# Kernel tuning notes

Hardware: AMD Instinct MI355X
Metric: run time of the kernel (lower is better)

## Reference

```python
import jax, jax.numpy as jnp
import numpy as np
import math

N_HEAD = 16


def setup_inputs() -> dict:
    key = jax.random.key(0)
    ks = jax.random.split(key, 4)
    B, S, D = 4, 2048, 1024
    x = jax.random.normal(ks[0], (B, S, D), dtype=jnp.float32)
    c_attn_w = jax.random.normal(ks[1], (D, 3 * D), dtype=jnp.float32) * 0.02
    c_attn_b = jnp.zeros((3 * D,), dtype=jnp.float32)
    c_proj_w = jax.random.normal(ks[2], (D, D), dtype=jnp.float32) * 0.02
    c_proj_b = jnp.zeros((D,), dtype=jnp.float32)
    # causal mask: True where attention is disallowed (future positions)
    mask_self_attention = jnp.triu(jnp.ones((S, S), dtype=bool), k=1)[None, None]
    return {"x": x, "c_attn_w": c_attn_w, "c_attn_b": c_attn_b,
            "c_proj_w": c_proj_w, "c_proj_b": c_proj_b,
            "mask_self_attention": mask_self_attention}


def reference(x, c_attn_w, c_attn_b, c_proj_w, c_proj_b, mask_self_attention):
    B, S, D = x.shape
    H = N_HEAD
    hd = D // H
    qkv = x @ c_attn_w + c_attn_b                      # [B,S,3D]
    q, k, v = jnp.split(qkv, 3, axis=-1)
    # split heads -> [B,H,S,hd]
    q = q.reshape(B, S, H, hd).transpose(0, 2, 1, 3)
    k = k.reshape(B, S, H, hd).transpose(0, 2, 1, 3)
    v = v.reshape(B, S, H, hd).transpose(0, 2, 1, 3)
    w = jnp.einsum('bhqd,bhkd->bhqk', q, k) / math.sqrt(hd)  # scale=True
    w = jnp.where(mask_self_attention, jnp.float32(-10000.0), w)
    w = jax.nn.softmax(w, axis=-1)
    a = jnp.einsum('bhqk,bhkd->bhqd', w, v)            # [B,H,S,hd]
    a = a.transpose(0, 2, 1, 3).reshape(B, S, D)       # merge heads
    return a @ c_proj_w + c_proj_b
```

## Files before the change

### kernel.cpp

```cpp
#include <hip/hip_runtime.h>
#include <cstdint>
#include <cstddef>

#define S_LEN 2048
#define D_MODEL 1024
#define HD 64

typedef __attribute__((ext_vector_type(8))) __bf16 bf16x8;
typedef __attribute__((ext_vector_type(8))) unsigned short u16x8;
typedef __attribute__((ext_vector_type(4))) float f32x4;
typedef __attribute__((ext_vector_type(4))) unsigned short u16x4;

static __device__ __forceinline__ unsigned short f32_bf16(float f) {
    unsigned int u = __float_as_uint(f);
    u += 0x7fffu + ((u >> 16) & 1u);
    return (unsigned short)(u >> 16);
}

static __device__ __forceinline__ unsigned short f32_bf16_rn(float f) {
    return __builtin_bit_cast(unsigned short, (__bf16)f);
}

static __device__ __forceinline__ float fast_exp2(float x) {
#if __has_builtin(__builtin_amdgcn_exp2f)
    return __builtin_amdgcn_exp2f(x);
#else
    float r; asm("v_exp_f32 %0, %1" : "=v"(r) : "v"(x)); return r;
#endif
}

static __device__ __forceinline__ void gload_lds16(const void* g, void* l) {
    __builtin_amdgcn_global_load_lds(
        (const __attribute__((address_space(1))) unsigned int*)g,
        (__attribute__((address_space(3))) unsigned int*)l,
        16, 0, 0);
}

static __device__ __forceinline__ bf16x8 frag8(const unsigned short* p) {
    return __builtin_bit_cast(bf16x8, *(const u16x8*)p);
}

__global__ void prep_k(const float* __restrict__ x, unsigned short* __restrict__ xb,
                       const float* __restrict__ caw, unsigned short* __restrict__ wqt,
                       const float* __restrict__ cpw, unsigned short* __restrict__ wpt)
{
    __shared__ float tile[32][33];
    const int blk = blockIdx.x;
    const int tid = threadIdx.x;
    if (blk < 8192) {
        int i = blk * 256 + tid;
        f32x4 v = ((const f32x4*)x)[i];
        u16x4 o;
        o[0] = f32_bf16(v[0]); o[1] = f32_bf16(v[1]);
        o[2] = f32_bf16(v[2]); o[3] = f32_bf16(v[3]);
        ((u16x4*)xb)[i] = o;
        return;
    }
    const float* in; unsigned short* out; int R, C, bx, by;
    if (blk < 11264) {
        int t = blk - 8192; in = caw; out = wqt; R = 1024; C = 3072;
        bx = t % 96; by = t / 96;
    } else {
        int t = blk - 11264; in = cpw; out = wpt; R = 1024; C = 1024;
        bx = t & 31; by = t >> 5;
    }
    int tx = tid & 31, ty = tid >> 5;
    int x0 = bx * 32, y0 = by * 32;
#pragma unroll
    for (int p = 0; p < 32; p += 8)
        tile[ty + p][tx] = in[(size_t)(y0 + ty + p) * C + x0 + tx];
    __syncthreads();
#pragma unroll
    for (int p = 0; p < 32; p += 8)
        out[(size_t)(x0 + ty + p) * R + y0 + tx] = f32_bf16(tile[tx][ty + p]);
}

__device__ __forceinline__ void gemm128_mainloop(
    const unsigned short* __restrict__ A,
    const unsigned short* __restrict__ Bt,
    unsigned short* As, unsigned short* Bs,
    int m0, int n0, int Kdim, f32x4 acc[][4])
{
    const int tid = threadIdx.x;
    const int lane = tid & 63, wave = tid >> 6;
    const int wm = wave & 1, wn = wave >> 1;
    const int quad = lane >> 4, l15 = lane & 15;
    const int srow = wave * 8 + (lane >> 3);
    const int scol = ((lane & 7) ^ (lane >> 3)) * 8;
    const unsigned short* Ag = A + (size_t)(m0 + srow) * Kdim + scol;
    const unsigned short* Bg = Bt + (size_t)(n0 + srow) * Kdim + scol;
    unsigned short* Asw = As + (wave * 8) * 64 + lane * 8;
    unsigned short* Bsw = Bs + (wave * 8) * 64 + lane * 8;
    const int mkey = l15 & 7;

    for (int k0 = 0; k0 < Kdim; k0 += 64) {
        __syncthreads();
#pragma unroll
        for (int p = 0; p < 4; ++p)
            gload_lds16(Ag + (size_t)(p * 32) * Kdim + k0, Asw + (p * 32) * 64);
#pragma unroll
        for (int p = 0; p < 4; ++p)
            gload_lds16(Bg + (size_t)(p * 32) * Kdim + k0, Bsw + (p * 32) * 64);
        __syncthreads();
#pragma unroll
        for (int kh = 0; kh < 2; ++kh) {
            bf16x8 af[4], bfv[4];
#pragma unroll
            for (int i = 0; i < 4; ++i)
                af[i] = frag8(As + (wm * 64 + i * 16 + l15) * 64 +
                              ((((kh << 2) + quad) ^ mkey) << 3));
#pragma unroll
            for (int j = 0; j < 4; ++j)
                bfv[j] = frag8(Bs + (wn * 64 + j * 16 + l15) * 64 +
                               ((((kh << 2) + quad) ^ mkey) << 3));
#pragma unroll
            for (int i = 0; i < 4; ++i)
#pragma unroll
                for (int j = 0; j < 4; ++j)
                    acc[i][j] = __builtin_amdgcn_mfma_f32_16x16x32_bf16(
                        af[i], bfv[j], acc[i][j], 0, 0, 0);
        }
    }
}

__global__ __launch_bounds__(256, 2) void gemm_qkv_k(
    const unsigned short* __restrict__ xb,
    const unsigned short* __restrict__ wt,
    const float* __restrict__ bias,
    unsigned short* __restrict__ q,
    unsigned short* __restrict__ k2,
    unsigned short* __restrict__ vt)
{
    __shared__ unsigned short Sh[128 * 132];
    unsigned short* As = Sh;
    unsigned short* Bs = Sh + 128 * 64;
    const int lin = blockIdx.x + 24 * blockIdx.y;
    const int swz = (lin & 7) * 192 + (lin >> 3);
    const int n0 = (swz % 24) * 128, m0 = (swz / 24) * 128;
    f32x4 acc[4][4] = {};
    gemm128_mainloop(xb, wt, As, Bs, m0, n0, 1024, acc);

    const int tid = threadIdx.x;
    const int lane = tid & 63, wave = tid >> 6;
    const int wm = wave & 1, wn = wave >> 1;
    const int quad = lane >> 4, l15 = lane & 15;
    const bool isq = (n0 < 1024);
    const bool isv = (n0 >= 2048);
    const int cb = n0 & 1023;

    if (!isv) {
        unsigned short* outp = isq ? q : k2;
#pragma unroll
        for (int j = 0; j < 4; ++j) {
            int ct = cb + wn * 64 + j * 16 + l15;
            int h = ct >> 6, d = ct & 63;
            float bv = bias[n0 + wn * 64 + j * 16 + l15];
#pragma unroll
            for (int i = 0; i < 4; ++i)
#pragma unroll
                for (int r = 0; r < 4; ++r) {
                    int row = m0 + wm * 64 + i * 16 + quad * 4 + r;
                    int bb = row >> 11, s = row & 2047;
                    float val = acc[i][j][r] + bv;
                    if (isq) val *= 0.1803368801111244f;
                    outp[((size_t)(bb * 16 + h) * S_LEN + s) * HD + d] = f32_bf16(val);
                }
        }
    } else {
        __syncthreads();
#pragma unroll
        for (int j = 0; j < 4; ++j) {
            float bv = bias[n0 + wn * 64 + j * 16 + l15];
            int lc = wn * 64 + j * 16 + l15;
#pragma unroll
            for (int i = 0; i < 4; ++i)
#pragma unroll
                for (int r = 0; r < 4; ++r) {
                    int lr = wm * 64 + i * 16 + quad * 4 + r;
                    Sh[lr * 132 + lc] = f32_bf16(acc[i][j][r] + bv);
                }
        }
        __syncthreads();
        const int lc = (tid & 63) + (wave & 1) * 64;
        const int sh2 = wave >> 1;
        const int bb = m0 >> 11;
        const int s0 = (m0 & 2047) + sh2 * 64;
        const int bh = bb * 16 + (cb >> 6) + (lc >> 6);
        unsigned short* vp = vt + ((size_t)bh * HD + (lc & 63)) * S_LEN + s0;
#pragma unroll
        for (int k8 = 0; k8 < 8; ++k8) {
            u16x8 w;
#pragma unroll
            for (int e = 0; e < 8; ++e)
                w[e] = Sh[(sh2 * 64 + k8 * 8 + e) * 132 + lc];
            *(u16x8*)(vp + k8 * 8) = w;
        }
    }
}

__global__ __launch_bounds__(256, 2) void gemm_proj_k(
    const unsigned short* __restrict__ am,
    const unsigned short* __restrict__ wpt,
    const float* __restrict__ bias,
    float* __restrict__ out)
{
    __shared__ unsigned short As[128 * 64], Bs[128 * 64];
    const int lin = blockIdx.x + 8 * blockIdx.y;
    const int swz = (lin & 7) * 64 + (lin >> 3);
    const int n0 = (swz % 8) * 128, m0 = (swz / 8) * 128;
    f32x4 acc[4][4] = {};
    gemm128_mainloop(am, wpt, As, Bs, m0, n0, 1024, acc);

    const int lane = threadIdx.x & 63, wave = threadIdx.x >> 6;
    const int wm = wave & 1, wn = wave >> 1;
    const int quad = lane >> 4, l15 = lane & 15;
#pragma unroll
    for (int j = 0; j < 4; ++j) {
        int col = n0 + wn * 64 + j * 16 + l15;
        float bv = bias[col];
#pragma unroll
        for (int i = 0; i < 4; ++i)
#pragma unroll
            for (int r = 0; r < 4; ++r) {
                int row = m0 + wm * 64 + i * 16 + quad * 4 + r;
                out[(size_t)row * 1024 + col] = acc[i][j][r] + bv;
            }
    }
}

#define PSTR 72
__global__ __launch_bounds__(256, 2) void flash_attn_k(
    const unsigned short* __restrict__ Q,
    const unsigned short* __restrict__ K,
    const unsigned short* __restrict__ Vt,
    unsigned short* __restrict__ Am)
{
    __shared__ unsigned short PsA[4 * 32 * PSTR];
    __shared__ unsigned short PsB[4 * 32 * PSTR];
    __shared__ unsigned short Ks[2][64 * 64];
    __shared__ unsigned short Vs[2][64 * 64];

    const int bid = blockIdx.x;
    const int w = (bid & 7) * 64 + (bid >> 3);
    const int bh = w >> 3;
    const int p = w & 7;
    const int qtA = p, qtB = 15 - p;
    const int b = bh >> 4, h = bh & 15;
    const int tid = threadIdx.x;
    const int lane = tid & 63, wave = tid >> 6;
    const int quad = lane >> 4, l15 = lane & 15;

    const size_t bh_off = (size_t)bh * S_LEN * HD;
    const unsigned short* Kg = K + bh_off;
    const unsigned short* Vtg = Vt + (size_t)bh * HD * S_LEN;

    const int lrow = (lane >> 3) & 7;
    const int scol = ((lane & 7) ^ lrow) * 8;
    const int srow = wave * 8 + lrow;
    const int ldst = (wave * 8) * 64 + lane * 8;

    bf16x8 qaA[2][2], qaB[2][2];
#pragma unroll
    for (int i = 0; i < 2; ++i)
#pragma unroll
        for (int kk = 0; kk < 2; ++kk) {
            qaA[i][kk] = frag8(Q + bh_off +
                (size_t)(qtA * 128 + wave * 32 + i * 16 + l15) * HD + kk * 32 + quad * 8);
            qaB[i][kk] = frag8(Q + bh_off +
                (size_t)(qtB * 128 + wave * 32 + i * 16 + l15) * HD + kk * 32 + quad * 8);
        }

    f32x4 oaccA[2][4] = {}, oaccB[2][4] = {};
    f32x4 laccA[2] = {}, laccB[2] = {};
    u16x8 ones_u = {0x3F80, 0x3F80, 0x3F80, 0x3F80, 0x3F80, 0x3F80, 0x3F80, 0x3F80};
    bf16x8 vone = __builtin_bit_cast(bf16x8, ones_u);

    const int q_baseA = qtA * 128 + wave * 32;
    const int q_baseB = qtB * 128 + wave * 32;
    const int nst  = 2 * qtB + 2;
    const int nstA = 2 * qtA + 2;
    const int wskip = (wave < 2) ? 1 : 0;
    const int nstB_w = nst - wskip;
    const int nstA_w = nstA - wskip;
    unsigned short* pwA = PsA + wave * (32 * PSTR);
    unsigned short* pwB = PsB + wave * (32 * PSTR);
    const int pkey = (l15 >> 2) & 3;
    const int kvkey = l15 & 7;

#pragma unroll
    for (int pp = 0; pp < 2; ++pp) {
        gload_lds16(Kg + (size_t)(srow + pp * 32) * HD + scol,
                    &Ks[0][ldst + (pp * 32) * 64]);
        gload_lds16(Vtg + (size_t)(srow + pp * 32) * S_LEN + scol,
                    &Vs[0][ldst + (pp * 32) * 64]);
    }
    __syncthreads();

    int cur = 0;
    for (int st = 0; st < nst; ++st) {
        if (st + 1 < nst) {
            const int nx = cur ^ 1;
            const size_t kroff = (size_t)((st + 1) * 64);
#pragma unroll
            for (int pp = 0; pp < 2; ++pp) {
                gload_lds16(Kg + (kroff + srow + pp * 32) * HD + scol,
                            &Ks[nx][ldst + (pp * 32) * 64]);
                gload_lds16(Vtg + (size_t)(srow + pp * 32) * S_LEN + kroff + scol,
                            &Vs[nx][ldst + (pp * 32) * 64]);
            }
        }
        const unsigned short* ksc = &Ks[cur][0];
        const unsigned short* vsc = &Vs[cur][0];
        const bool actA = (st < nstA_w);
        const bool actB = (st < nstB_w);

        if (actB) {
            f32x4 saccA[2][4] = {}, saccB[2][4] = {};
            __builtin_amdgcn_s_setprio(1);
#pragma unroll
            for (int kk = 0; kk < 2; ++kk) {
                bf16x8 kb[4];
#pragma unroll
                for (int j = 0; j < 4; ++j)
                    kb[j] = frag8(ksc + (j * 16 + l15) * 64 +
                                  ((((kk << 2) + quad) ^ kvkey) << 3));
#pragma unroll
                for (int i = 0; i < 2; ++i)
#pragma unroll
                    for (int j = 0; j < 4; ++j)
                        saccB[i][j] = __builtin_amdgcn_mfma_f32_16x16x32_bf16(
                            qaB[i][kk], kb[j], saccB[i][j], 0, 0, 0);
                if (actA) {
#pragma unroll
                    for (int i = 0; i < 2; ++i)
#pragma unroll
                        for (int j = 0; j < 4; ++j)
                            saccA[i][j] = __builtin_amdgcn_mfma_f32_16x16x32_bf16(
                                qaA[i][kk], kb[j], saccA[i][j], 0, 0, 0);
                }
            }
            __builtin_amdgcn_s_setprio(0);

            if (st * 64 + 63 > q_baseB) {
#pragma unroll
                for (int i = 0; i < 2; ++i)
#pragma unroll
                    for (int j = 0; j < 4; ++j)
#pragma unroll
                        for (int r = 0; r < 4; ++r) {
                            int kg = st * 64 + j * 16 + l15;
                            int qg = q_baseB + i * 16 + quad * 4 + r;
                            if (kg > qg) saccB[i][j][r] = -__builtin_inff();
                        }
            }
            if (actA && st * 64 + 63 > q_baseA) {
#pragma unroll
                for (int i = 0; i < 2; ++i)
#pragma unroll
                    for (int j = 0; j < 4; ++j)
#pragma unroll
                        for (int r = 0; r < 4; ++r) {
                            int kg = st * 64 + j * 16 + l15;
                            int qg = q_baseA + i * 16 + quad * 4 + r;
                            if (kg > qg) saccA[i][j][r] = -__builtin_inff();
                        }
            }

#pragma unroll
            for (int i = 0; i < 2; ++i)
#pragma unroll
                for (int j = 0; j < 4; ++j) {
                    int cs = ((j ^ quad) << 4) + l15;
#pragma unroll
                    for (int r = 0; r < 4; ++r)
                        pwB[(i * 16 + quad * 4 + r) * PSTR + cs] =
                            f32_bf16_rn(fast_exp2(saccB[i][j][r]));
                }
            if (actA) {
#pragma unroll
                for (int i = 0; i < 2; ++i)
#pragma unroll
                    for (int j = 0; j < 4; ++j) {
                        int cs = ((j ^ quad) << 4) + l15;
#pragma unroll
                        for (int r = 0; r < 4; ++r)
                            pwA[(i * 16 + quad * 4 + r) * PSTR + cs] =
                                f32_bf16_rn(fast_exp2(saccA[i][j][r]));
                    }
            }

#pragma unroll
            for (int kk = 0; kk < 2; ++kk) {
                bf16x8 vb[4];
#pragma unroll
                for (int d4 = 0; d4 < 4; ++d4)
                    vb[d4] = frag8(vsc + (d4 * 16 + l15) * 64 +
                                   ((((kk << 2) + quad) ^ kvkey) << 3));
                const int coff = ((((kk << 1) + (quad >> 1)) ^ pkey) << 4) + ((quad & 1) << 3);

                bf16x8 paB[2];
#pragma unroll
                for (int i = 0; i < 2; ++i)
                    paB[i] = frag8(pwB + (i * 16 + l15) * PSTR + coff);
                __builtin_amdgcn_s_setprio(1);
#pragma unroll
                for (int d4 = 0; d4 < 4; ++d4)
#pragma unroll
                    for (int i = 0; i < 2; ++i)
                        oaccB[i][d4] = __builtin_amdgcn_mfma_f32_16x16x32_bf16(
                            paB[i], vb[d4], oaccB[i][d4], 0, 0, 0);
#pragma unroll
                for (int i = 0; i < 2; ++i)
                    laccB[i] = __builtin_amdgcn_mfma_f32_16x16x32_bf16(
                        paB[i], vone, laccB[i], 0, 0, 0);
                __builtin_amdgcn_s_setprio(0);

                if (actA) {
                    bf16x8 paA[2];
#pragma unroll
                    for (int i = 0; i < 2; ++i)
                        paA[i] = frag8(pwA + (i * 16 + l15) * PSTR + coff);
                    __builtin_amdgcn_s_setprio(1);
#pragma unroll
                    for (int d4 = 0; d4 < 4; ++d4)
#pragma unroll
                        for (int i = 0; i < 2; ++i)
                            oaccA[i][d4] = __builtin_amdgcn_mfma_f32_16x16x32_bf16(
                                paA[i], vb[d4], oaccA[i][d4], 0, 0, 0);
#pragma unroll
                    for (int i = 0; i < 2; ++i)
                        laccA[i] = __builtin_amdgcn_mfma_f32_16x16x32_bf16(
                            paA[i], vone, laccA[i], 0, 0, 0);
                    __builtin_amdgcn_s_setprio(0);
                }
            }
        }

        __syncthreads();
        cur ^= 1;
    }

    unsigned short* AmpB = Am + ((size_t)(b * S_LEN + q_baseB)) * D_MODEL + h * 64;
#pragma unroll
    for (int i = 0; i < 2; ++i)
#pragma unroll
        for (int r = 0; r < 4; ++r) {
            float inv = 1.f / laccB[i][r];
            int qloc = i * 16 + quad * 4 + r;
#pragma unroll
            for (int d4 = 0; d4 < 4; ++d4)
                AmpB[(size_t)qloc * D_MODEL + d4 * 16 + l15] =
                    f32_bf16_rn(oaccB[i][d4][r] * inv);
        }
    unsigned short* AmpA = Am + ((size_t)(b * S_LEN + q_baseA)) * D_MODEL + h * 64;
#pragma unroll
    for (int i = 0; i < 2; ++i)
#pragma unroll
        for (int r = 0; r < 4; ++r) {
            float inv = 1.f / laccA[i][r];
            int qloc = i * 16 + quad * 4 + r;
#pragma unroll
            for (int d4 = 0; d4 < 4; ++d4)
                AmpA[(size_t)qloc * D_MODEL + d4 * 16 + l15] =
                    f32_bf16_rn(oaccA[i][d4][r] * inv);
        }
}

extern "C" void kernel_launch(void* const* d_in, const int* in_sizes, int n_in,
                              void* d_out, int out_size, void* d_ws, size_t ws_size,
                              hipStream_t stream)
{
    const float* x = (const float*)d_in[0];
    const float* c_attn_w = (const float*)d_in[1];
    const float* c_attn_b = (const float*)d_in[2];
    const float* c_proj_w = (const float*)d_in[3];
    const float* c_proj_b = (const float*)d_in[4];
    float* out = (float*)d_out;

    char* ws = (char*)d_ws;
    unsigned short* xb  = (unsigned short*)(ws);
    unsigned short* q   = (unsigned short*)(ws + 16777216);
    unsigned short* k   = (unsigned short*)(ws + 33554432);
    unsigned short* vt  = (unsigned short*)(ws + 67108864);
    unsigned short* wqt = (unsigned short*)(ws + 83886080);
    unsigned short* wpt = (unsigned short*)(ws + 90177536);

    prep_k<<<12288, 256, 0, stream>>>(x, xb, c_attn_w, wqt, c_proj_w, wpt);
    gemm_qkv_k<<<dim3(24, 64), 256, 0, stream>>>(xb, wqt, c_attn_b, q, k, vt);
    flash_attn_k<<<512, 256, 0, stream>>>(q, k, vt, xb );
    gemm_proj_k<<<dim3(8, 64), 256, 0, stream>>>(xb , wpt, c_proj_b, out);
}
```

Measured before the change: 260.9 us.

## Split paired-tile attention blocks into one query tile per block

```diff
diff --git a/kernel.cpp b/kernel.cpp
--- a/kernel.cpp
+++ b/kernel.cpp
@@ -229,22 +229,21 @@
 }
 
 #define PSTR 72
-__global__ __launch_bounds__(256, 2) void flash_attn_k(
+__global__ __launch_bounds__(256, 3) void flash_attn_k(
     const unsigned short* __restrict__ Q,
     const unsigned short* __restrict__ K,
     const unsigned short* __restrict__ Vt,
     unsigned short* __restrict__ Am)
 {
-    __shared__ unsigned short PsA[4 * 32 * PSTR];
-    __shared__ unsigned short PsB[4 * 32 * PSTR];
+    __shared__ unsigned short Ps[4 * 32 * PSTR];
     __shared__ unsigned short Ks[2][64 * 64];
     __shared__ unsigned short Vs[2][64 * 64];
 
     const int bid = blockIdx.x;
-    const int w = (bid & 7) * 64 + (bid >> 3);
-    const int bh = w >> 3;
-    const int p = w & 7;
-    const int qtA = p, qtB = 15 - p;
+    const int xcd = bid & 7;
+    const int w = bid >> 3;
+    const int qt = 15 - (w >> 3);
+    const int bh = xcd * 8 + (w & 7);
     const int b = bh >> 4, h = bh & 15;
     const int tid = threadIdx.x;
     const int lane = tid & 63, wave = tid >> 6;
@@ -259,31 +258,24 @@
     const int srow = wave * 8 + lrow;
     const int ldst = (wave * 8) * 64 + lane * 8;
 
-    bf16x8 qaA[2][2], qaB[2][2];
+    const int q_base = qt * 128 + wave * 32;
+
+    bf16x8 qa[2][2];
 #pragma unroll
     for (int i = 0; i < 2; ++i)
 #pragma unroll
-        for (int kk = 0; kk < 2; ++kk) {
-            qaA[i][kk] = frag8(Q + bh_off +
-                (size_t)(qtA * 128 + wave * 32 + i * 16 + l15) * HD + kk * 32 + quad * 8);
-            qaB[i][kk] = frag8(Q + bh_off +
-                (size_t)(qtB * 128 + wave * 32 + i * 16 + l15) * HD + kk * 32 + quad * 8);
-        }
-
-    f32x4 oaccA[2][4] = {}, oaccB[2][4] = {};
-    f32x4 laccA[2] = {}, laccB[2] = {};
+        for (int kk = 0; kk < 2; ++kk)
+            qa[i][kk] = frag8(Q + bh_off +
+                (size_t)(q_base + i * 16 + l15) * HD + kk * 32 + quad * 8);
+
+    f32x4 oacc[2][4] = {};
+    f32x4 lacc[2] = {};
     u16x8 ones_u = {0x3F80, 0x3F80, 0x3F80, 0x3F80, 0x3F80, 0x3F80, 0x3F80, 0x3F80};
     bf16x8 vone = __builtin_bit_cast(bf16x8, ones_u);
 
-    const int q_baseA = qtA * 128 + wave * 32;
-    const int q_baseB = qtB * 128 + wave * 32;
-    const int nst  = 2 * qtB + 2;
-    const int nstA = 2 * qtA + 2;
-    const int wskip = (wave < 2) ? 1 : 0;
-    const int nstB_w = nst - wskip;
-    const int nstA_w = nstA - wskip;
-    unsigned short* pwA = PsA + wave * (32 * PSTR);
-    unsigned short* pwB = PsB + wave * (32 * PSTR);
+    const int nst = 2 * qt + 2;
+    const int nst_w = nst - ((wave < 2) ? 1 : 0);
+    unsigned short* pw = Ps + wave * (32 * PSTR);
     const int pkey = (l15 >> 2) & 3;
     const int kvkey = l15 & 7;
 
@@ -311,11 +303,9 @@
         }
         const unsigned short* ksc = &Ks[cur][0];
         const unsigned short* vsc = &Vs[cur][0];
-        const bool actA = (st < nstA_w);
-        const bool actB = (st < nstB_w);
-
-        if (actB) {
-            f32x4 saccA[2][4] = {}, saccB[2][4] = {};
+
+        if (st < nst_w) {
+            f32x4 sacc[2][4] = {};
             __builtin_amdgcn_s_setprio(1);
 #pragma unroll
             for (int kk = 0; kk < 2; ++kk) {
@@ -328,20 +318,12 @@
                 for (int i = 0; i < 2; ++i)
 #pragma unroll
                     for (int j = 0; j < 4; ++j)
-                        saccB[i][j] = __builtin_amdgcn_mfma_f32_16x16x32_bf16(
-                            qaB[i][kk], kb[j], saccB[i][j], 0, 0, 0);
-                if (actA) {
-#pragma unroll
-                    for (int i = 0; i < 2; ++i)
-#pragma unroll
-                        for (int j = 0; j < 4; ++j)
-                            saccA[i][j] = __builtin_amdgcn_mfma_f32_16x16x32_bf16(
-                                qaA[i][kk], kb[j], saccA[i][j], 0, 0, 0);
-                }
+                        sacc[i][j] = __builtin_amdgcn_mfma_f32_16x16x32_bf16(
+                            qa[i][kk], kb[j], sacc[i][j], 0, 0, 0);
             }
             __builtin_amdgcn_s_setprio(0);
 
-            if (st * 64 + 63 > q_baseB) {
+            if (st * 64 + 63 > q_base) {
 #pragma unroll
                 for (int i = 0; i < 2; ++i)
 #pragma unroll
@@ -349,22 +331,10 @@
 #pragma unroll
                         for (int r = 0; r < 4; ++r) {
                             int kg = st * 64 + j * 16 + l15;
-                            int qg = q_baseB + i * 16 + quad * 4 + r;
-                            if (kg > qg) saccB[i][j][r] = -__builtin_inff();
+                            int qg = q_base + i * 16 + quad * 4 + r;
+                            if (kg > qg) sacc[i][j][r] = -__builtin_inff();
                         }
             }
-            if (actA && st * 64 + 63 > q_baseA) {
-#pragma unroll
-                for (int i = 0; i < 2; ++i)
-#pragma unroll
-                    for (int j = 0; j < 4; ++j)
-#pragma unroll
-                        for (int r = 0; r < 4; ++r) {
-                            int kg = st * 64 + j * 16 + l15;
-                            int qg = q_baseA + i * 16 + quad * 4 + r;
-                            if (kg > qg) saccA[i][j][r] = -__builtin_inff();
-                        }
-            }
 
 #pragma unroll
             for (int i = 0; i < 2; ++i)
@@ -373,21 +343,9 @@
                     int cs = ((j ^ quad) << 4) + l15;
 #pragma unroll
                     for (int r = 0; r < 4; ++r)
-                        pwB[(i * 16 + quad * 4 + r) * PSTR + cs] =
-                            f32_bf16_rn(fast_exp2(saccB[i][j][r]));
+                        pw[(i * 16 + quad * 4 + r) * PSTR + cs] =
+                            f32_bf16_rn(fast_exp2(sacc[i][j][r]));
                 }
-            if (actA) {
-#pragma unroll
-                for (int i = 0; i < 2; ++i)
-#pragma unroll
-                    for (int j = 0; j < 4; ++j) {
-                        int cs = ((j ^ quad) << 4) + l15;
-#pragma unroll
-                        for (int r = 0; r < 4; ++r)
-                            pwA[(i * 16 + quad * 4 + r) * PSTR + cs] =
-                                f32_bf16_rn(fast_exp2(saccA[i][j][r]));
-                    }
-            }
 
 #pragma unroll
             for (int kk = 0; kk < 2; ++kk) {
@@ -398,41 +356,22 @@
                                    ((((kk << 2) + quad) ^ kvkey) << 3));
                 const int coff = ((((kk << 1) + (quad >> 1)) ^ pkey) << 4) + ((quad & 1) << 3);
 
-                bf16x8 paB[2];
+                bf16x8 pa[2];
 #pragma unroll
                 for (int i = 0; i < 2; ++i)
-                    paB[i] = frag8(pwB + (i * 16 + l15) * PSTR + coff);
+                    pa[i] = frag8(pw + (i * 16 + l15) * PSTR + coff);
                 __builtin_amdgcn_s_setprio(1);
 #pragma unroll
                 for (int d4 = 0; d4 < 4; ++d4)
 #pragma unroll
                     for (int i = 0; i < 2; ++i)
-                        oaccB[i][d4] = __builtin_amdgcn_mfma_f32_16x16x32_bf16(
-                            paB[i], vb[d4], oaccB[i][d4], 0, 0, 0);
+                        oacc[i][d4] = __builtin_amdgcn_mfma_f32_16x16x32_bf16(
+                            pa[i], vb[d4], oacc[i][d4], 0, 0, 0);
 #pragma unroll
                 for (int i = 0; i < 2; ++i)
-                    laccB[i] = __builtin_amdgcn_mfma_f32_16x16x32_bf16(
-                        paB[i], vone, laccB[i], 0, 0, 0);
+                    lacc[i] = __builtin_amdgcn_mfma_f32_16x16x32_bf16(
+                        pa[i], vone, lacc[i], 0, 0, 0);
                 __builtin_amdgcn_s_setprio(0);
-
-                if (actA) {
-                    bf16x8 paA[2];
-#pragma unroll
-                    for (int i = 0; i < 2; ++i)
-                        paA[i] = frag8(pwA + (i * 16 + l15) * PSTR + coff);
-                    __builtin_amdgcn_s_setprio(1);
-#pragma unroll
-                    for (int d4 = 0; d4 < 4; ++d4)
-#pragma unroll
-                        for (int i = 0; i < 2; ++i)
-                            oaccA[i][d4] = __builtin_amdgcn_mfma_f32_16x16x32_bf16(
-                                paA[i], vb[d4], oaccA[i][d4], 0, 0, 0);
-#pragma unroll
-                    for (int i = 0; i < 2; ++i)
-                        laccA[i] = __builtin_amdgcn_mfma_f32_16x16x32_bf16(
-                            paA[i], vone, laccA[i], 0, 0, 0);
-                    __builtin_amdgcn_s_setprio(0);
-                }
             }
         }
 
@@ -440,29 +379,17 @@
         cur ^= 1;
     }
 
-    unsigned short* AmpB = Am + ((size_t)(b * S_LEN + q_baseB)) * D_MODEL + h * 64;
+    unsigned short* Amp = Am + ((size_t)(b * S_LEN + q_base)) * D_MODEL + h * 64;
 #pragma unroll
     for (int i = 0; i < 2; ++i)
 #pragma unroll
         for (int r = 0; r < 4; ++r) {
-            float inv = 1.f / laccB[i][r];
+            float inv = 1.f / lacc[i][r];
             int qloc = i * 16 + quad * 4 + r;
 #pragma unroll
             for (int d4 = 0; d4 < 4; ++d4)
-                AmpB[(size_t)qloc * D_MODEL + d4 * 16 + l15] =
-                    f32_bf16_rn(oaccB[i][d4][r] * inv);
-        }
-    unsigned short* AmpA = Am + ((size_t)(b * S_LEN + q_baseA)) * D_MODEL + h * 64;
-#pragma unroll
-    for (int i = 0; i < 2; ++i)
-#pragma unroll
-        for (int r = 0; r < 4; ++r) {
-            float inv = 1.f / laccA[i][r];
-            int qloc = i * 16 + quad * 4 + r;
-#pragma unroll
-            for (int d4 = 0; d4 < 4; ++d4)
-                AmpA[(size_t)qloc * D_MODEL + d4 * 16 + l15] =
-                    f32_bf16_rn(oaccA[i][d4][r] * inv);
+                Amp[(size_t)qloc * D_MODEL + d4 * 16 + l15] =
+                    f32_bf16_rn(oacc[i][d4][r] * inv);
         }
 }
 
@@ -487,6 +414,6 @@
 
     prep_k<<<12288, 256, 0, stream>>>(x, xb, c_attn_w, wqt, c_proj_w, wpt);
     gemm_qkv_k<<<dim3(24, 64), 256, 0, stream>>>(xb, wqt, c_attn_b, q, k, vt);
-    flash_attn_k<<<512, 256, 0, stream>>>(q, k, vt, xb );
+    flash_attn_k<<<1024, 256, 0, stream>>>(q, k, vt, xb );
     gemm_proj_k<<<dim3(8, 64), 256, 0, stream>>>(xb , wpt, c_proj_b, out);
 }
```

Result: faster. 246.2 us (median of 2 runs) (-5.6%).
